# Kernel optimization log

Measured on AMD Instinct MI355X. Metric: run time of the kernel, lower is better.

## Reference

```python
import jax, jax.numpy as jnp
import numpy as np

H = 51  # hidden size hard-coded in the module

def lstm_cell(x, h, c, W_ih, W_hh, b_ih, b_hh):
    # PyTorch LSTMCell: gates = x @ W_ih^T + b_ih + h @ W_hh^T + b_hh
    g = x @ W_ih.T + h @ W_hh.T + (b_ih + b_hh)  # [B, 4H]
    i, f, gg, o = jnp.split(g, 4, axis=-1)
    c_new = jax.nn.sigmoid(f) * c + jax.nn.sigmoid(i) * jnp.tanh(gg)
    h_new = jax.nn.sigmoid(o) * jnp.tanh(c_new)
    return h_new, c_new

def setup_inputs() -> dict:
    key = jax.random.key(0)
    ks = jax.random.split(key, 12)
    B, T = 2048, 2048
    s1 = 1.0 / np.sqrt(H)
    u = lambda k, shape: jax.random.uniform(k, shape, jnp.float32, -s1, s1)
    return {
        "input": jax.random.normal(ks[0], (B, T), jnp.float32),
        "W_ih1": u(ks[1], (4 * H, 1)),
        "W_hh1": u(ks[2], (4 * H, H)),
        "b_ih1": u(ks[3], (4 * H,)),
        "b_hh1": u(ks[4], (4 * H,)),
        "W_ih2": u(ks[5], (4 * H, H)),
        "W_hh2": u(ks[6], (4 * H, H)),
        "b_ih2": u(ks[7], (4 * H,)),
        "b_hh2": u(ks[8], (4 * H,)),
        "W_lin": u(ks[9], (1, H)),
        "b_lin": u(ks[10], (1,)),
    }

def reference(input, W_ih1, W_hh1, b_ih1, b_hh1, W_ih2, W_hh2, b_ih2, b_hh2, W_lin, b_lin):
    B, T = input.shape
    xs = input.T[:, :, None]  # [T, B, 1]
    h1 = jnp.zeros((B, H), input.dtype)
    c1 = jnp.zeros((B, H), input.dtype)
    h2 = jnp.zeros((B, H), input.dtype)
    c2 = jnp.zeros((B, H), input.dtype)

    def step(carry, x_t):
        h1, c1, h2, c2 = carry
        h1, c1 = lstm_cell(x_t, h1, c1, W_ih1, W_hh1, b_ih1, b_hh1)
        h2, c2 = lstm_cell(h1, h2, c2, W_ih2, W_hh2, b_ih2, b_hh2)
        y = h2 @ W_lin.T + b_lin  # [B, 1]
        return (h1, c1, h2, c2), y[:, 0]

    _, ys = jax.lax.scan(step, (h1, c1, h2, c2), xs)  # ys: [T, B]
    return ys.T  # [B, T]
```

## Files before the change

kernel.cpp:

```cpp
#include <hip/hip_runtime.h>

#define H 51
#define TSEQ 2048
#define BB 16
#define THREADS 1024

typedef _Float16 __attribute__((ext_vector_type(8))) half8;
typedef float    __attribute__((ext_vector_type(4))) float4v;

#define LOG2E    1.44269504f
#define TWOLOG2E 2.88539008f

__device__ __forceinline__ float lstm_ew(float4v a, float& c) {
    float eA = __builtin_amdgcn_exp2f(-a[0]);
    float eB = __builtin_amdgcn_exp2f(a[2]);
    float eF = __builtin_amdgcn_exp2f(-a[1]);
    float pA = eA + 1.0f, pB = eB + 1.0f, pF = eF + 1.0f;
    float dAB = pA * pB;
    float num = fmaf(c, dAB, (eB - 1.0f) * pF);
    float r   = __builtin_amdgcn_rcpf(dAB * pF);
    float cn  = num * r;
    c = cn;
    float uD = fminf(cn * TWOLOG2E, 126.0f);
    float eD = __builtin_amdgcn_exp2f(uD);
    float eC = __builtin_amdgcn_exp2f(-a[3]);
    float r2 = __builtin_amdgcn_rcpf((eC + 1.0f) * (eD + 1.0f));
    return (eD - 1.0f) * r2;
}

__global__ __launch_bounds__(THREADS)
void lstm_w16b_kernel(const float* __restrict__ input,
                      const float* __restrict__ W_ih1, const float* __restrict__ W_hh1,
                      const float* __restrict__ b_ih1, const float* __restrict__ b_hh1,
                      const float* __restrict__ W_ih2, const float* __restrict__ W_hh2,
                      const float* __restrict__ b_ih2, const float* __restrict__ b_hh2,
                      const float* __restrict__ W_lin, const float* __restrict__ b_lin,
                      float* __restrict__ out)
{
    __shared__ half8 hb1[2][2][64];
    __shared__ half8 hb2[2][2][64];
    __shared__ float xss[2][64 * 17];
    __shared__ float ybf[128][17];

    const int tid  = threadIdx.x;
    const int wv   = tid >> 6;
    const int lane = tid & 63;
    const int n    = lane & 15;
    const int qd   = lane >> 4;
    const int b0   = blockIdx.x * BB;
    const float blin = b_lin[0];

    if (tid < 256) {
        half8 z = {0,0,0,0,0,0,0,0};
        (&hb1[0][0][0])[tid] = z;
        (&hb2[0][0][0])[tid] = z;
    }

    if (wv == 15) {
#pragma unroll
        for (int k = 0; k < 16; ++k)
            xss[0][lane * 17 + k] = input[(size_t)(b0 + k) * TSEQ + lane];
    }

    half8 wa1[2];
    half8 wa2[4];
    {
        const int tw1 = (wv < 12) ? wv : ((wv == 13) ? 12 : 13);
        const int tw2 = (wv < 12) ? wv : ((wv == 14) ? 12 : 13);
        {
            const int arow = tw1 * 16 + n;
            const int cell = arow >> 2, gate = arow & 3;
            const int orow = gate * H + cell;
            const float gsc = (gate == 2) ? TWOLOG2E : LOG2E;
            const bool rok = (arow < 4 * H);
#pragma unroll
            for (int s = 0; s < 2; ++s)
#pragma unroll
                for (int j = 0; j < 8; ++j) {
                    int kk = s * 32 + qd * 8 + j;
                    wa1[s][j] = (_Float16)((rok && kk < H) ? gsc * W_hh1[orow * H + kk] : 0.f);
                }
        }
        {
            const int arow = tw2 * 16 + n;
            const int cell = arow >> 2, gate = arow & 3;
            const int orow = gate * H + cell;
            const float gsc = (gate == 2) ? TWOLOG2E : LOG2E;
            const bool rok = (arow < 4 * H);
#pragma unroll
            for (int s = 0; s < 4; ++s)
#pragma unroll
                for (int j = 0; j < 8; ++j) {
                    int kk = s * 32 + qd * 8 + j;
                    float w = 0.f;
                    if (rok) {
                        if (kk < H)                       w = gsc * W_ih2[orow * H + kk];
                        else if (kk >= 64 && kk < 64 + H) w = gsc * W_hh2[orow * H + (kk - 64)];
                    } else if (arow == 204) {
                        if (kk >= 64 && kk < 64 + H)      w = W_lin[kk - 64];
                    }
                    wa2[s][j] = (_Float16)w;
                }
        }
    }

    const int ewv = (wv == 13 || wv == 14) ? 12 : ((wv < 12) ? wv : 13);
    const int jj  = ewv * 4 + qd;
    float4v bias1v, wih1v, bias2v;
    {
        const bool cok1 = (jj < H) && (wv < 12 || wv == 13);
        const bool cok2 = (jj < H) && (wv < 12 || wv == 14);
#pragma unroll
        for (int r = 0; r < 4; ++r) {
            const float gsc = (r == 2) ? TWOLOG2E : LOG2E;
            const int orow = r * H + jj;
            bias1v[r] = cok1 ? gsc * (b_ih1[orow] + b_hh1[orow]) : 0.f;
            wih1v[r]  = cok1 ? gsc * W_ih1[orow] : 0.f;
            bias2v[r] = cok2 ? gsc * (b_ih2[orow] + b_hh2[orow]) : 0.f;
        }
    }

    float c1 = 0.f, c2 = 0.f;
    const int js = jj >> 5, jq = (jj & 31) >> 3, j7 = jj & 7;

    __syncthreads();

    if (wv < 12 || wv == 13) {
        const float xb = xss[0][n];
        float4v a;
#pragma unroll
        for (int r = 0; r < 4; ++r) a[r] = fmaf(wih1v[r], xb, bias1v[r]);
        float h = lstm_ew(a, c1);
        ((_Float16*)&hb1[0][js][jq * 16 + n])[j7] = (_Float16)h;
    }
    __syncthreads();

#define STEP(t, P)                                                              \
    {                                                                           \
        if (wv < 12) {                                                          \
            __builtin_amdgcn_s_setprio(1);                                      \
            half8 g1[2], g2[2];                                                 \
            g1[0] = hb1[P][0][lane];      g1[1] = hb1[P][1][lane];              \
            g2[0] = hb2[P ^ 1][0][lane];  g2[1] = hb2[P ^ 1][1][lane];          \
                      \
            const int t1 = (t) + 1;                                             \
            const float xb = xss[(t1 >> 6) & 1][(t1 & 63) * 17 + n];            \
            float4v a1;                                                         \
            _Pragma("unroll")                                                   \
            for (int r = 0; r < 4; ++r) a1[r] = fmaf(wih1v[r], xb, bias1v[r]);  \
            a1 = __builtin_amdgcn_mfma_f32_16x16x32_f16(wa1[0], g1[0], a1, 0, 0, 0); \
            a1 = __builtin_amdgcn_mfma_f32_16x16x32_f16(wa1[1], g1[1], a1, 0, 0, 0); \
            float4v a2a = bias2v;                                               \
            float4v a2b = (float4v){0.f, 0.f, 0.f, 0.f};                        \
            a2a = __builtin_amdgcn_mfma_f32_16x16x32_f16(wa2[0], g1[0], a2a, 0, 0, 0); \
            a2b = __builtin_amdgcn_mfma_f32_16x16x32_f16(wa2[2], g2[0], a2b, 0, 0, 0); \
            a2a = __builtin_amdgcn_mfma_f32_16x16x32_f16(wa2[1], g1[1], a2a, 0, 0, 0); \
            a2b = __builtin_amdgcn_mfma_f32_16x16x32_f16(wa2[3], g2[1], a2b, 0, 0, 0); \
                                          \
            {                                                                   \
                float h = lstm_ew(a1, c1);                                      \
                ((_Float16*)&hb1[P ^ 1][js][jq * 16 + n])[j7] = (_Float16)h;    \
            }                                                                   \
                                                             \
            {                                                                   \
                float4v a2;                                                     \
                _Pragma("unroll")                                               \
                for (int r = 0; r < 4; ++r) a2[r] = a2a[r] + a2b[r];            \
                float h = lstm_ew(a2, c2);                                      \
                ((_Float16*)&hb2[P][js][jq * 16 + n])[j7] = (_Float16)h;        \
            }                                                                   \
            __builtin_amdgcn_s_setprio(0);                                      \
        } else if (wv == 12) {                                                  \
             \
             \
            if ((t) > 64 && ((t) & 63) == 1) {                                  \
                const int tb = (t) - 65;                                        \
                const int sb = tb & 127;                                        \
                _Pragma("unroll")                                               \
                for (int r = 0; r < BB; ++r)                                    \
                    out[(size_t)(b0 + r) * TSEQ + tb + lane] = ybf[sb + lane][r]; \
            }                                                                   \
        } else if (wv == 13) {                                                  \
                 \
            __builtin_amdgcn_s_setprio(1);                                      \
            half8 g1[2];                                                        \
            g1[0] = hb1[P][0][lane];      g1[1] = hb1[P][1][lane];              \
            const int t1 = (t) + 1;                                             \
            const float xb = xss[(t1 >> 6) & 1][(t1 & 63) * 17 + n];            \
            float4v a1;                                                         \
            _Pragma("unroll")                                                   \
            for (int r = 0; r < 4; ++r) a1[r] = fmaf(wih1v[r], xb, bias1v[r]);  \
            a1 = __builtin_amdgcn_mfma_f32_16x16x32_f16(wa1[0], g1[0], a1, 0, 0, 0); \
            a1 = __builtin_amdgcn_mfma_f32_16x16x32_f16(wa1[1], g1[1], a1, 0, 0, 0); \
            float h = lstm_ew(a1, c1);                                          \
            ((_Float16*)&hb1[P ^ 1][js][jq * 16 + n])[j7] = (_Float16)h;        \
            __builtin_amdgcn_s_setprio(0);                                      \
        } else if (wv == 14) {                                                  \
                       \
            __builtin_amdgcn_s_setprio(1);                                      \
            half8 g1[2], g2[2];                                                 \
            g1[0] = hb1[P][0][lane];      g1[1] = hb1[P][1][lane];              \
            g2[0] = hb2[P ^ 1][0][lane];  g2[1] = hb2[P ^ 1][1][lane];          \
            float4v a2a = bias2v;                                               \
            float4v a2b = (float4v){0.f, 0.f, 0.f, 0.f};                        \
            a2a = __builtin_amdgcn_mfma_f32_16x16x32_f16(wa2[0], g1[0], a2a, 0, 0, 0); \
            a2b = __builtin_amdgcn_mfma_f32_16x16x32_f16(wa2[2], g2[0], a2b, 0, 0, 0); \
            a2a = __builtin_amdgcn_mfma_f32_16x16x32_f16(wa2[1], g1[1], a2a, 0, 0, 0); \
            a2b = __builtin_amdgcn_mfma_f32_16x16x32_f16(wa2[3], g2[1], a2b, 0, 0, 0); \
            float4v a2;                                                         \
            _Pragma("unroll")                                                   \
            for (int r = 0; r < 4; ++r) a2[r] = a2a[r] + a2b[r];                \
            float h = lstm_ew(a2, c2);                                          \
            ((_Float16*)&hb2[P][js][jq * 16 + n])[j7] = (_Float16)h;            \
            if (qd == 3) ybf[((t) - 1) & 127][n] = a2[0] + blin;    \
            __builtin_amdgcn_s_setprio(0);                                      \
        } else {                                                                \
                                       \
            if (((t) & 63) == 32 && (t) + 32 < TSEQ) {                          \
                const int cp = ((t) >> 6) & 1;                                  \
                _Pragma("unroll")                                               \
                for (int k = 0; k < 16; ++k)                                    \
                    xss[cp ^ 1][lane * 17 + k] =                                \
                        input[(size_t)(b0 + k) * TSEQ + ((t) + 32) + lane];     \
            }                                                                   \
        }                                                                       \
        __syncthreads();                                                        \
    }

#pragma unroll 1
    for (int t = 0; t < TSEQ; t += 2) {
        STEP(t, 0)
        STEP(t + 1, 1)
    }
#undef STEP

    if (wv == 14) {
        half8 g2a = hb2[1][0][lane], g2b = hb2[1][1][lane];
        float4v yb = (float4v){0.f, 0.f, 0.f, 0.f};
        yb = __builtin_amdgcn_mfma_f32_16x16x32_f16(wa2[2], g2a, yb, 0, 0, 0);
        yb = __builtin_amdgcn_mfma_f32_16x16x32_f16(wa2[3], g2b, yb, 0, 0, 0);
        if (qd == 3) ybf[127][n] = yb[0] + blin;
    }
    __syncthreads();
    if (wv == 12) {
        const int tb = TSEQ - 64;
#pragma unroll
        for (int r = 0; r < BB; ++r)
            out[(size_t)(b0 + r) * TSEQ + tb + lane] = ybf[64 + lane][r];
    }
}

extern "C" void kernel_launch(void* const* d_in, const int* in_sizes, int n_in,
                              void* d_out, int out_size, void* d_ws, size_t ws_size,
                              hipStream_t stream) {
    const float* input = (const float*)d_in[0];
    const float* W_ih1 = (const float*)d_in[1];
    const float* W_hh1 = (const float*)d_in[2];
    const float* b_ih1 = (const float*)d_in[3];
    const float* b_hh1 = (const float*)d_in[4];
    const float* W_ih2 = (const float*)d_in[5];
    const float* W_hh2 = (const float*)d_in[6];
    const float* b_ih2 = (const float*)d_in[7];
    const float* b_hh2 = (const float*)d_in[8];
    const float* W_lin = (const float*)d_in[9];
    const float* b_lin = (const float*)d_in[10];

    lstm_w16b_kernel<<<dim3(2048 / BB), dim3(THREADS), 0, stream>>>(
        input, W_ih1, W_hh1, b_ih1, b_hh1,
        W_ih2, W_hh2, b_ih2, b_hh2, W_lin, b_lin,
        (float*)d_out);
}
```

Before: 1.420 ms.

## Halve block to 8 waves, each compute wave handling three gate tiles

Work is redistributed so each block uses 512 threads: four compute waves each process three 16-row gate tiles for both LSTM layers, and separate waves handle the tail tiles, the output drain and the input prefetch. The aim is cheaper per-step __syncthreads barriers and per-wave instruction-level parallelism from interleaving three independent MFMA chains, in exchange for more serial work per wave on the critical path of each timestep. Register pressure grows with three copies of the weights, biases and cell states, and the s_setprio hints are dropped.

```diff
diff --git a/kernel.cpp b/kernel.cpp
--- a/kernel.cpp
+++ b/kernel.cpp
@@ -3,7 +3,7 @@
 #define H 51
 #define TSEQ 2048
 #define BB 16
-#define THREADS 1024
+#define THREADS 512
 
 typedef _Float16 __attribute__((ext_vector_type(8))) half8;
 typedef float    __attribute__((ext_vector_type(4))) float4v;
@@ -29,13 +29,13 @@
 }
 
 __global__ __launch_bounds__(THREADS)
-void lstm_w16b_kernel(const float* __restrict__ input,
-                      const float* __restrict__ W_ih1, const float* __restrict__ W_hh1,
-                      const float* __restrict__ b_ih1, const float* __restrict__ b_hh1,
-                      const float* __restrict__ W_ih2, const float* __restrict__ W_hh2,
-                      const float* __restrict__ b_ih2, const float* __restrict__ b_hh2,
-                      const float* __restrict__ W_lin, const float* __restrict__ b_lin,
-                      float* __restrict__ out)
+void lstm_w8_kernel(const float* __restrict__ input,
+                    const float* __restrict__ W_ih1, const float* __restrict__ W_hh1,
+                    const float* __restrict__ b_ih1, const float* __restrict__ b_hh1,
+                    const float* __restrict__ W_ih2, const float* __restrict__ W_hh2,
+                    const float* __restrict__ b_ih2, const float* __restrict__ b_hh2,
+                    const float* __restrict__ W_lin, const float* __restrict__ b_lin,
+                    float* __restrict__ out)
 {
     __shared__ half8 hb1[2][2][64];
     __shared__ half8 hb2[2][2][64];
@@ -56,123 +56,155 @@
         (&hb2[0][0][0])[tid] = z;
     }
 
-    if (wv == 15) {
+    if (wv == 7) {
 #pragma unroll
         for (int k = 0; k < 16; ++k)
             xss[0][lane * 17 + k] = input[(size_t)(b0 + k) * TSEQ + lane];
     }
 
-    half8 wa1[2];
-    half8 wa2[4];
-    {
-        const int tw1 = (wv < 12) ? wv : ((wv == 13) ? 12 : 13);
-        const int tw2 = (wv < 12) ? wv : ((wv == 14) ? 12 : 13);
-        {
-            const int arow = tw1 * 16 + n;
-            const int cell = arow >> 2, gate = arow & 3;
-            const int orow = gate * H + cell;
-            const float gsc = (gate == 2) ? TWOLOG2E : LOG2E;
-            const bool rok = (arow < 4 * H);
-#pragma unroll
-            for (int s = 0; s < 2; ++s)
-#pragma unroll
-                for (int j = 0; j < 8; ++j) {
-                    int kk = s * 32 + qd * 8 + j;
-                    wa1[s][j] = (_Float16)((rok && kk < H) ? gsc * W_hh1[orow * H + kk] : 0.f);
+    int tl[3];
+    tl[0] = (wv < 4) ? wv : ((wv == 4 || wv == 5) ? 12 : 13);
+    tl[1] = (wv < 4) ? wv + 4 : 13;
+    tl[2] = (wv < 4) ? wv + 8 : 13;
+
+    half8 wa1[3][2];
+    half8 wa2[3][4];
+    float4v bias1v[3], wih1v[3], bias2v[3];
+    int jsv[3], jqv[3], j7v[3];
+#pragma unroll
+    for (int m = 0; m < 3; ++m) {
+        const int tile = tl[m];
+        const int arow = tile * 16 + n;
+        const int cell = arow >> 2, gate = arow & 3;
+        const int orow = gate * H + cell;
+        const float gsc = (gate == 2) ? TWOLOG2E : LOG2E;
+        const bool rok = (arow < 4 * H);
+#pragma unroll
+        for (int s = 0; s < 2; ++s)
+#pragma unroll
+            for (int j = 0; j < 8; ++j) {
+                int kk = s * 32 + qd * 8 + j;
+                wa1[m][s][j] = (_Float16)((rok && kk < H) ? gsc * W_hh1[orow * H + kk] : 0.f);
+            }
+#pragma unroll
+        for (int s = 0; s < 4; ++s)
+#pragma unroll
+            for (int j = 0; j < 8; ++j) {
+                int kk = s * 32 + qd * 8 + j;
+                float w = 0.f;
+                if (rok) {
+                    if (kk < H)                       w = gsc * W_ih2[orow * H + kk];
+                    else if (kk >= 64 && kk < 64 + H) w = gsc * W_hh2[orow * H + (kk - 64)];
+                } else if (arow == 204) {
+                    if (kk >= 64 && kk < 64 + H)      w = W_lin[kk - 64];
                 }
+                wa2[m][s][j] = (_Float16)w;
+            }
+        const int jj = tile * 4 + qd;
+        jsv[m] = jj >> 5; jqv[m] = (jj & 31) >> 3; j7v[m] = jj & 7;
+        const bool cok = (jj < H);
+#pragma unroll
+        for (int r = 0; r < 4; ++r) {
+            const float gsc2 = (r == 2) ? TWOLOG2E : LOG2E;
+            const int orow2 = r * H + jj;
+            bias1v[m][r] = cok ? gsc2 * (b_ih1[orow2] + b_hh1[orow2]) : 0.f;
+            wih1v[m][r]  = cok ? gsc2 * W_ih1[orow2] : 0.f;
+            bias2v[m][r] = cok ? gsc2 * (b_ih2[orow2] + b_hh2[orow2]) : 0.f;
         }
-        {
-            const int arow = tw2 * 16 + n;
-            const int cell = arow >> 2, gate = arow & 3;
-            const int orow = gate * H + cell;
-            const float gsc = (gate == 2) ? TWOLOG2E : LOG2E;
-            const bool rok = (arow < 4 * H);
-#pragma unroll
-            for (int s = 0; s < 4; ++s)
-#pragma unroll
-                for (int j = 0; j < 8; ++j) {
-                    int kk = s * 32 + qd * 8 + j;
-                    float w = 0.f;
-                    if (rok) {
-                        if (kk < H)                       w = gsc * W_ih2[orow * H + kk];
-                        else if (kk >= 64 && kk < 64 + H) w = gsc * W_hh2[orow * H + (kk - 64)];
-                    } else if (arow == 204) {
-                        if (kk >= 64 && kk < 64 + H)      w = W_lin[kk - 64];
-                    }
-                    wa2[s][j] = (_Float16)w;
-                }
+    }
+
+    float c1[3] = {0.f, 0.f, 0.f}, c2[3] = {0.f, 0.f, 0.f};
+
+    __syncthreads();
+
+    if (wv < 4) {
+        const float xb = xss[0][n];
+#pragma unroll
+        for (int m = 0; m < 3; ++m) {
+            float4v a;
+#pragma unroll
+            for (int r = 0; r < 4; ++r) a[r] = fmaf(wih1v[m][r], xb, bias1v[m][r]);
+            float h = lstm_ew(a, c1[m]);
+            ((_Float16*)&hb1[0][jsv[m]][jqv[m] * 16 + n])[j7v[m]] = (_Float16)h;
         }
-    }
-
-    const int ewv = (wv == 13 || wv == 14) ? 12 : ((wv < 12) ? wv : 13);
-    const int jj  = ewv * 4 + qd;
-    float4v bias1v, wih1v, bias2v;
-    {
-        const bool cok1 = (jj < H) && (wv < 12 || wv == 13);
-        const bool cok2 = (jj < H) && (wv < 12 || wv == 14);
-#pragma unroll
-        for (int r = 0; r < 4; ++r) {
-            const float gsc = (r == 2) ? TWOLOG2E : LOG2E;
-            const int orow = r * H + jj;
-            bias1v[r] = cok1 ? gsc * (b_ih1[orow] + b_hh1[orow]) : 0.f;
-            wih1v[r]  = cok1 ? gsc * W_ih1[orow] : 0.f;
-            bias2v[r] = cok2 ? gsc * (b_ih2[orow] + b_hh2[orow]) : 0.f;
-        }
-    }
-
-    float c1 = 0.f, c2 = 0.f;
-    const int js = jj >> 5, jq = (jj & 31) >> 3, j7 = jj & 7;
-
-    __syncthreads();
-
-    if (wv < 12 || wv == 13) {
+    } else if (wv == 4) {
         const float xb = xss[0][n];
         float4v a;
 #pragma unroll
-        for (int r = 0; r < 4; ++r) a[r] = fmaf(wih1v[r], xb, bias1v[r]);
-        float h = lstm_ew(a, c1);
-        ((_Float16*)&hb1[0][js][jq * 16 + n])[j7] = (_Float16)h;
+        for (int r = 0; r < 4; ++r) a[r] = fmaf(wih1v[0][r], xb, bias1v[0][r]);
+        float h = lstm_ew(a, c1[0]);
+        ((_Float16*)&hb1[0][jsv[0]][jqv[0] * 16 + n])[j7v[0]] = (_Float16)h;
     }
     __syncthreads();
 
 #define STEP(t, P)                                                              \
     {                                                                           \
-        if (wv < 12) {                                                          \
-            __builtin_amdgcn_s_setprio(1);                                      \
+        if (wv < 4) {                                                           \
             half8 g1[2], g2[2];                                                 \
             g1[0] = hb1[P][0][lane];      g1[1] = hb1[P][1][lane];              \
             g2[0] = hb2[P ^ 1][0][lane];  g2[1] = hb2[P ^ 1][1][lane];          \
-                      \
+            const int t1 = (t) + 1;                                             \
+            const float xb = xss[(t1 >> 6) & 1][(t1 & 63) * 17 + n];            \
+            float4v a1v[3], a2v[3];                                             \
+            _Pragma("unroll")                                                   \
+            for (int m = 0; m < 3; ++m) {                                       \
+                float4v a1;                                                     \
+                _Pragma("unroll")                                               \
+                for (int r = 0; r < 4; ++r) a1[r] = fmaf(wih1v[m][r], xb, bias1v[m][r]); \
+                a1 = __builtin_amdgcn_mfma_f32_16x16x32_f16(wa1[m][0], g1[0], a1, 0, 0, 0); \
+                a1 = __builtin_amdgcn_mfma_f32_16x16x32_f16(wa1[m][1], g1[1], a1, 0, 0, 0); \
+                a1v[m] = a1;                                                    \
+            }                                                                   \
+            _Pragma("unroll")                                                   \
+            for (int m = 0; m < 3; ++m) {                                       \
+                float4v a2a = bias2v[m];                                        \
+                float4v a2b = (float4v){0.f, 0.f, 0.f, 0.f};                    \
+                a2a = __builtin_amdgcn_mfma_f32_16x16x32_f16(wa2[m][0], g1[0], a2a, 0, 0, 0); \
+                a2b = __builtin_amdgcn_mfma_f32_16x16x32_f16(wa2[m][2], g2[0], a2b, 0, 0, 0); \
+                a2a = __builtin_amdgcn_mfma_f32_16x16x32_f16(wa2[m][1], g1[1], a2a, 0, 0, 0); \
+                a2b = __builtin_amdgcn_mfma_f32_16x16x32_f16(wa2[m][3], g2[1], a2b, 0, 0, 0); \
+                a2v[m] = a2a + a2b;                                             \
+            }                                                                   \
+            _Pragma("unroll")                                                   \
+            for (int m = 0; m < 3; ++m) {                                       \
+                float h = lstm_ew(a1v[m], c1[m]);                               \
+                ((_Float16*)&hb1[P ^ 1][jsv[m]][jqv[m] * 16 + n])[j7v[m]] = (_Float16)h; \
+            }                                                                   \
+            _Pragma("unroll")                                                   \
+            for (int m = 0; m < 3; ++m) {                                       \
+                float h = lstm_ew(a2v[m], c2[m]);                               \
+                ((_Float16*)&hb2[P][jsv[m]][jqv[m] * 16 + n])[j7v[m]] = (_Float16)h; \
+            }                                                                   \
+        } else if (wv == 4) {                                                   \
+                             \
+            half8 g1[2];                                                        \
+            g1[0] = hb1[P][0][lane];      g1[1] = hb1[P][1][lane];              \
             const int t1 = (t) + 1;                                             \
             const float xb = xss[(t1 >> 6) & 1][(t1 & 63) * 17 + n];            \
             float4v a1;                                                         \
             _Pragma("unroll")                                                   \
-            for (int r = 0; r < 4; ++r) a1[r] = fmaf(wih1v[r], xb, bias1v[r]);  \
-            a1 = __builtin_amdgcn_mfma_f32_16x16x32_f16(wa1[0], g1[0], a1, 0, 0, 0); \
-            a1 = __builtin_amdgcn_mfma_f32_16x16x32_f16(wa1[1], g1[1], a1, 0, 0, 0); \
-            float4v a2a = bias2v;                                               \
+            for (int r = 0; r < 4; ++r) a1[r] = fmaf(wih1v[0][r], xb, bias1v[0][r]); \
+            a1 = __builtin_amdgcn_mfma_f32_16x16x32_f16(wa1[0][0], g1[0], a1, 0, 0, 0); \
+            a1 = __builtin_amdgcn_mfma_f32_16x16x32_f16(wa1[0][1], g1[1], a1, 0, 0, 0); \
+            float h = lstm_ew(a1, c1[0]);                                       \
+            ((_Float16*)&hb1[P ^ 1][jsv[0]][jqv[0] * 16 + n])[j7v[0]] = (_Float16)h; \
+        } else if (wv == 5) {                                                   \
+                       \
+            half8 g1[2], g2[2];                                                 \
+            g1[0] = hb1[P][0][lane];      g1[1] = hb1[P][1][lane];              \
+            g2[0] = hb2[P ^ 1][0][lane];  g2[1] = hb2[P ^ 1][1][lane];          \
+            float4v a2a = bias2v[0];                                            \
             float4v a2b = (float4v){0.f, 0.f, 0.f, 0.f};                        \
-            a2a = __builtin_amdgcn_mfma_f32_16x16x32_f16(wa2[0], g1[0], a2a, 0, 0, 0); \
-            a2b = __builtin_amdgcn_mfma_f32_16x16x32_f16(wa2[2], g2[0], a2b, 0, 0, 0); \
-            a2a = __builtin_amdgcn_mfma_f32_16x16x32_f16(wa2[1], g1[1], a2a, 0, 0, 0); \
-            a2b = __builtin_amdgcn_mfma_f32_16x16x32_f16(wa2[3], g2[1], a2b, 0, 0, 0); \
-                                          \
-            {                                                                   \
-                float h = lstm_ew(a1, c1);                                      \
-                ((_Float16*)&hb1[P ^ 1][js][jq * 16 + n])[j7] = (_Float16)h;    \
-            }                                                                   \
-                                                             \
-            {                                                                   \
-                float4v a2;                                                     \
-                _Pragma("unroll")                                               \
-                for (int r = 0; r < 4; ++r) a2[r] = a2a[r] + a2b[r];            \
-                float h = lstm_ew(a2, c2);                                      \
-                ((_Float16*)&hb2[P][js][jq * 16 + n])[j7] = (_Float16)h;        \
-            }                                                                   \
-            __builtin_amdgcn_s_setprio(0);                                      \
-        } else if (wv == 12) {                                                  \
-             \
-             \
+            a2a = __builtin_amdgcn_mfma_f32_16x16x32_f16(wa2[0][0], g1[0], a2a, 0, 0, 0); \
+            a2b = __builtin_amdgcn_mfma_f32_16x16x32_f16(wa2[0][2], g2[0], a2b, 0, 0, 0); \
+            a2a = __builtin_amdgcn_mfma_f32_16x16x32_f16(wa2[0][1], g1[1], a2a, 0, 0, 0); \
+            a2b = __builtin_amdgcn_mfma_f32_16x16x32_f16(wa2[0][3], g2[1], a2b, 0, 0, 0); \
+            float4v a2 = a2a + a2b;                                             \
+            float h = lstm_ew(a2, c2[0]);                                       \
+            ((_Float16*)&hb2[P][jsv[0]][jqv[0] * 16 + n])[j7v[0]] = (_Float16)h; \
+            if (qd == 3) ybf[((t) - 1) & 127][n] = a2[0] + blin;    \
+        } else if (wv == 6) {                                                   \
+                    \
             if ((t) > 64 && ((t) & 63) == 1) {                                  \
                 const int tb = (t) - 65;                                        \
                 const int sb = tb & 127;                                        \
@@ -180,42 +212,8 @@
                 for (int r = 0; r < BB; ++r)                                    \
                     out[(size_t)(b0 + r) * TSEQ + tb + lane] = ybf[sb + lane][r]; \
             }                                                                   \
-        } else if (wv == 13) {                                                  \
-                 \
-            __builtin_amdgcn_s_setprio(1);                                      \
-            half8 g1[2];                                                        \
-            g1[0] = hb1[P][0][lane];      g1[1] = hb1[P][1][lane];              \
-            const int t1 = (t) + 1;                                             \
-            const float xb = xss[(t1 >> 6) & 1][(t1 & 63) * 17 + n];            \
-            float4v a1;                                                         \
-            _Pragma("unroll")                                                   \
-            for (int r = 0; r < 4; ++r) a1[r] = fmaf(wih1v[r], xb, bias1v[r]);  \
-            a1 = __builtin_amdgcn_mfma_f32_16x16x32_f16(wa1[0], g1[0], a1, 0, 0, 0); \
-            a1 = __builtin_amdgcn_mfma_f32_16x16x32_f16(wa1[1], g1[1], a1, 0, 0, 0); \
-            float h = lstm_ew(a1, c1);                                          \
-            ((_Float16*)&hb1[P ^ 1][js][jq * 16 + n])[j7] = (_Float16)h;        \
-            __builtin_amdgcn_s_setprio(0);                                      \
-        } else if (wv == 14) {                                                  \
-                       \
-            __builtin_amdgcn_s_setprio(1);                                      \
-            half8 g1[2], g2[2];                                                 \
-            g1[0] = hb1[P][0][lane];      g1[1] = hb1[P][1][lane];              \
-            g2[0] = hb2[P ^ 1][0][lane];  g2[1] = hb2[P ^ 1][1][lane];          \
-            float4v a2a = bias2v;                                               \
-            float4v a2b = (float4v){0.f, 0.f, 0.f, 0.f};                        \
-            a2a = __builtin_amdgcn_mfma_f32_16x16x32_f16(wa2[0], g1[0], a2a, 0, 0, 0); \
-            a2b = __builtin_amdgcn_mfma_f32_16x16x32_f16(wa2[2], g2[0], a2b, 0, 0, 0); \
-            a2a = __builtin_amdgcn_mfma_f32_16x16x32_f16(wa2[1], g1[1], a2a, 0, 0, 0); \
-            a2b = __builtin_amdgcn_mfma_f32_16x16x32_f16(wa2[3], g2[1], a2b, 0, 0, 0); \
-            float4v a2;                                                         \
-            _Pragma("unroll")                                                   \
-            for (int r = 0; r < 4; ++r) a2[r] = a2a[r] + a2b[r];                \
-            float h = lstm_ew(a2, c2);                                          \
-            ((_Float16*)&hb2[P][js][jq * 16 + n])[j7] = (_Float16)h;            \
-            if (qd == 3) ybf[((t) - 1) & 127][n] = a2[0] + blin;    \
-            __builtin_amdgcn_s_setprio(0);                                      \
         } else {                                                                \
-                                       \
+                                        \
             if (((t) & 63) == 32 && (t) + 32 < TSEQ) {                          \
                 const int cp = ((t) >> 6) & 1;                                  \
                 _Pragma("unroll")                                               \
@@ -234,15 +232,15 @@
     }
 #undef STEP
 
-    if (wv == 14) {
+    if (wv == 5) {
         half8 g2a = hb2[1][0][lane], g2b = hb2[1][1][lane];
         float4v yb = (float4v){0.f, 0.f, 0.f, 0.f};
-        yb = __builtin_amdgcn_mfma_f32_16x16x32_f16(wa2[2], g2a, yb, 0, 0, 0);
-        yb = __builtin_amdgcn_mfma_f32_16x16x32_f16(wa2[3], g2b, yb, 0, 0, 0);
+        yb = __builtin_amdgcn_mfma_f32_16x16x32_f16(wa2[0][2], g2a, yb, 0, 0, 0);
+        yb = __builtin_amdgcn_mfma_f32_16x16x32_f16(wa2[0][3], g2b, yb, 0, 0, 0);
         if (qd == 3) ybf[127][n] = yb[0] + blin;
     }
     __syncthreads();
-    if (wv == 12) {
+    if (wv == 6) {
         const int tb = TSEQ - 64;
 #pragma unroll
         for (int r = 0; r < BB; ++r)
@@ -265,7 +263,7 @@
     const float* W_lin = (const float*)d_in[9];
     const float* b_lin = (const float*)d_in[10];
 
-    lstm_w16b_kernel<<<dim3(2048 / BB), dim3(THREADS), 0, stream>>>(
+    lstm_w8_kernel<<<dim3(2048 / BB), dim3(THREADS), 0, stream>>>(
         input, W_ih1, W_hh1, b_ih1, b_hh1,
         W_ih2, W_hh2, b_ih2, b_hh2, W_lin, b_lin,
         (float*)d_out);
```

After: 1.599 ms. +12.6%, slower.
